# Optimization experiments

Measured on AMD Instinct MI355X. Metric: run time of the kernel, lower is better.

Reference implementation:

```python
import jax, jax.numpy as jnp
import numpy as np

EPS_LN = 1e-6
EPS_BN = 1e-5
NUM_HEADS = 8


def _dwconv(img, w, b=None, stride=1):
    # img: (B,C,H,W), w: (C,1,k,k) depthwise
    out = jax.lax.conv_general_dilated(
        img, w, (stride, stride), 'SAME',
        feature_group_count=img.shape[1],
        dimension_numbers=('NCHW', 'OIHW', 'NCHW'))
    if b is not None:
        out = out + b[None, :, None, None]
    return out


def _layernorm(x, g, b):
    m = jnp.mean(x, axis=-1, keepdims=True)
    v = jnp.mean(jnp.square(x - m), axis=-1, keepdims=True)
    return (x - m) * jax.lax.rsqrt(v + EPS_LN) * g + b


def _hardswish(x):
    return x * jnp.clip(x + 3.0, 0.0, 6.0) * (1.0 / 6.0)


def _forward(img, domain_label, pe_dw_w, pe_pw_w, pe_bn_g, pe_bn_b, pe_bn_m, pe_bn_v,
             cpe_w, cpe_b, norm1_g, norm1_b, qkv_w, qkv_b,
             crpe_w3, crpe_b3, crpe_w5, crpe_b5, crpe_w7, crpe_b7,
             dom_w1, dom_b1, dom_w2, dom_b2, proj_w, proj_b,
             norm2_g, norm2_b, fc1_w, fc1_b, fc2_w, fc2_b, d):
    B = img.shape[0]
    # --- DWCPatchEmbed_M: depthwise 3x3 s2 + pointwise 1x1 + domain BN (eval) + hardswish ---
    x = _dwconv(img, pe_dw_w, None, stride=2)                      # (B,Cin,H,W)
    x = jax.lax.conv_general_dilated(x, pe_pw_w, (1, 1), 'SAME',
                                     dimension_numbers=('NCHW', 'OIHW', 'NCHW'))
    g, be, mu, var = pe_bn_g[d], pe_bn_b[d], pe_bn_m[d], pe_bn_v[d]
    scale_bn = g * jax.lax.rsqrt(var + EPS_BN)
    x = (x - mu[None, :, None, None]) * scale_bn[None, :, None, None] + be[None, :, None, None]
    x = _hardswish(x)
    _, C, H, W = x.shape
    N = H * W
    x = x.reshape(B, C, N).transpose(0, 2, 1)                      # (B,N,C) tokens

    # --- ConvPosEnc: depthwise 3x3 on image layout, residual ---
    img2 = x.transpose(0, 2, 1).reshape(B, C, H, W)
    x = x + _dwconv(img2, cpe_w, cpe_b).reshape(B, C, N).transpose(0, 2, 1)

    # --- FactorAtt_ConvRelPosEnc_Sup ---
    cur = _layernorm(x, norm1_g[d], norm1_b[d])
    h = NUM_HEADS
    Ch = C // h
    qkv = cur @ qkv_w + qkv_b                                      # (B,N,3C)
    qkv = qkv.reshape(B, N, 3, h, Ch).transpose(2, 0, 3, 1, 4)     # (3,B,h,N,Ch)
    q, k, v = qkv[0], qkv[1], qkv[2]
    k_sm = jax.nn.softmax(k, axis=2)                               # softmax over tokens
    kv = jnp.einsum('bhnk,bhnv->bhkv', k_sm, v)                    # (B,h,Ch,Ch)
    factor_att = jnp.einsum('bhnk,bhkv->bhnv', q, kv)              # (B,h,N,Ch)

    # conv relative position encoding: windows {3:2heads, 5:3heads, 7:3heads}
    v_img = v.transpose(0, 1, 3, 2).reshape(B, C, H, W)            # (B, h*Ch, H, W)
    s1, s2 = 2 * Ch, 5 * Ch
    cv = jnp.concatenate([
        _dwconv(v_img[:, :s1], crpe_w3, crpe_b3),
        _dwconv(v_img[:, s1:s2], crpe_w5, crpe_b5),
        _dwconv(v_img[:, s2:], crpe_w7, crpe_b7)], axis=1)
    cv = cv.reshape(B, h, Ch, N).transpose(0, 1, 3, 2)             # (B,h,N,Ch)
    crpe = q * cv

    factor_att = (Ch ** -0.5) * factor_att + crpe

    # domain gate: Linear->ReLU->Linear on one-hot, softmax over heads
    da = jax.nn.relu(domain_label @ dom_w1 + dom_b1) @ dom_w2 + dom_b2   # (B,C)
    da = da.reshape(B, h, Ch)[:, :, None, :]                        # (B,h,1,Ch)
    da = jax.nn.softmax(da, axis=1)
    out = da * factor_att                                           # (B,h,N,Ch)
    out = out.transpose(0, 2, 1, 3).reshape(B, N, C)
    out = out @ proj_w + proj_b
    x = x + out

    # --- MLP (ratio 8), domain LayerNorm, residual ---
    cur = _layernorm(x, norm2_g[d], norm2_b[d])
    cur = jax.nn.gelu(cur @ fc1_w + fc1_b, approximate=False) @ fc2_w + fc2_b
    x = x + cur
    return x


def setup_inputs() -> dict:
    key = jax.random.key(0)
    ks = jax.random.split(key, 16)
    B, Cin, Hin, Win = 8, 64, 128, 128
    C, h, D = 128, NUM_HEADS, 4
    Ch = C // h
    hid_dom = C // 2
    hid_mlp = 8 * C
    f = jnp.float32

    def n(k, shape, s=0.02):
        return (s * jax.random.normal(k, shape)).astype(f)

    img = jax.random.normal(ks[0], (B, Cin, Hin, Win), dtype=f)
    domain_label = jax.nn.one_hot(jnp.zeros((B,), jnp.int32), D, dtype=f)
    return dict(
        img=img, domain_label=domain_label,
        pe_dw_w=n(ks[1], (Cin, 1, 3, 3), 0.1),
        pe_pw_w=n(ks[2], (C, Cin, 1, 1), 0.1),
        pe_bn_g=jnp.ones((D, C), f), pe_bn_b=jnp.zeros((D, C), f),
        pe_bn_m=n(ks[3], (D, C), 0.1),
        pe_bn_v=jnp.ones((D, C), f),
        cpe_w=n(ks[4], (C, 1, 3, 3), 0.1), cpe_b=jnp.zeros((C,), f),
        norm1_g=jnp.ones((D, C), f), norm1_b=jnp.zeros((D, C), f),
        qkv_w=n(ks[5], (C, 3 * C)), qkv_b=jnp.zeros((3 * C,), f),
        crpe_w3=n(ks[6], (2 * Ch, 1, 3, 3), 0.1), crpe_b3=jnp.zeros((2 * Ch,), f),
        crpe_w5=n(ks[7], (3 * Ch, 1, 5, 5), 0.1), crpe_b5=jnp.zeros((3 * Ch,), f),
        crpe_w7=n(ks[8], (3 * Ch, 1, 7, 7), 0.1), crpe_b7=jnp.zeros((3 * Ch,), f),
        dom_w1=n(ks[9], (D, hid_dom)), dom_b1=jnp.zeros((hid_dom,), f),
        dom_w2=n(ks[10], (hid_dom, C)), dom_b2=jnp.zeros((C,), f),
        proj_w=n(ks[11], (C, C)), proj_b=jnp.zeros((C,), f),
        norm2_g=jnp.ones((D, C), f), norm2_b=jnp.zeros((D, C), f),
        fc1_w=n(ks[12], (C, hid_mlp)), fc1_b=jnp.zeros((hid_mlp,), f),
        fc2_w=n(ks[13], (hid_mlp, C)), fc2_b=jnp.zeros((C,), f),
        d=0,
    )


def reference(img, domain_label, pe_dw_w, pe_pw_w, pe_bn_g, pe_bn_b, pe_bn_m, pe_bn_v,
              cpe_w, cpe_b, norm1_g, norm1_b, qkv_w, qkv_b,
              crpe_w3, crpe_b3, crpe_w5, crpe_b5, crpe_w7, crpe_b7,
              dom_w1, dom_b1, dom_w2, dom_b2, proj_w, proj_b,
              norm2_g, norm2_b, fc1_w, fc1_b, fc2_w, fc2_b, d):
    return _forward(img, domain_label, pe_dw_w, pe_pw_w, pe_bn_g, pe_bn_b, pe_bn_m, pe_bn_v,
                    cpe_w, cpe_b, norm1_g, norm1_b, qkv_w, qkv_b,
                    crpe_w3, crpe_b3, crpe_w5, crpe_b5, crpe_w7, crpe_b7,
                    dom_w1, dom_b1, dom_w2, dom_b2, proj_w, proj_b,
                    norm2_g, norm2_b, fc1_w, fc1_b, fc2_w, fc2_b, d)
```

## Files before the change

kernel.cpp:

```cpp
#include <hip/hip_runtime.h>
#include <math.h>

#define EPS_LN 1e-6f
#define EPS_BN 1e-5f

typedef __attribute__((ext_vector_type(8))) short bf16x8;
typedef __attribute__((ext_vector_type(4))) float f32x4;

__device__ __forceinline__ float wave_reduce_sum(float v) {
    #pragma unroll
    for (int m = 32; m >= 1; m >>= 1) v += __shfl_xor(v, m, 64);
    return v;
}
__device__ __forceinline__ float wave_reduce_max(float v) {
    #pragma unroll
    for (int m = 32; m >= 1; m >>= 1) v = fmaxf(v, __shfl_xor(v, m, 64));
    return v;
}
__device__ __forceinline__ short f2bf(float f) {
    union { float f; unsigned u; } v; v.f = f;
    unsigned r = v.u + 0x7fff + ((v.u >> 16) & 1);
    return (short)(r >> 16);
}
__device__ __forceinline__ unsigned pack2bf(float a, float b) {
    return (unsigned)(unsigned short)f2bf(a) | ((unsigned)(unsigned short)f2bf(b) << 16);
}

__global__ __launch_bounds__(256) void pe_kernel(
    const float* __restrict__ img, const float* __restrict__ dww,
    const float* __restrict__ pww, const float* __restrict__ bn_g,
    const float* __restrict__ bn_b, const float* __restrict__ bn_m,
    const float* __restrict__ bn_v, const int* __restrict__ dptr,
    float* __restrict__ t1) {
    __shared__ float dw[64 * 68];
    __shared__ float wsm[64 * 132];
    int bx = blockIdx.x;
    int b = bx >> 6, y = bx & 63;
    int tid = threadIdx.x;
    int d = *dptr;

    for (int idx = tid; idx < 8192; idx += 256) {
        int co = idx >> 6, ci = idx & 63;
        wsm[ci * 132 + co] = pww[idx];
    }

    for (int it = 0; it < 4; ++it) {
        int task = tid + it * 256;
        int ci = task >> 4, xx0 = (task & 15) * 4;
        const float* ip = img + (size_t)(b * 64 + ci) * 16384;
        const float* wd = dww + ci * 9;
        float a0 = 0.f, a1 = 0.f, a2 = 0.f, a3 = 0.f;
        #pragma unroll
        for (int r = 0; r < 3; ++r) {
            int iy = 2 * y + r;
            if (iy >= 128) continue;
            const float* rp = ip + iy * 128 + 2 * xx0;
            float u[9];
            *(f32x4*)&u[0] = *(const f32x4*)rp;
            *(f32x4*)&u[4] = *(const f32x4*)(rp + 4);
            u[8] = (xx0 < 60) ? rp[8] : 0.f;
            #pragma unroll
            for (int s = 0; s < 3; ++s) {
                float w = wd[r * 3 + s];
                a0 += u[s] * w;
                a1 += u[2 + s] * w;
                a2 += u[4 + s] * w;
                a3 += u[6 + s] * w;
            }
        }
        f32x4 st = {a0, a1, a2, a3};
        *(f32x4*)&dw[ci * 68 + xx0] = st;
    }
    __syncthreads();

    int xg = tid & 15, cog = tid >> 4;
    int xx0 = xg * 4, co0 = cog * 8;
    f32x4 acc[8];
    f32x4 zr = {0.f, 0.f, 0.f, 0.f};
    #pragma unroll
    for (int i = 0; i < 8; ++i) acc[i] = zr;
    for (int ci = 0; ci < 64; ++ci) {
        f32x4 dv = *(const f32x4*)&dw[ci * 68 + xx0];
        f32x4 w0 = *(const f32x4*)&wsm[ci * 132 + co0];
        f32x4 w1 = *(const f32x4*)&wsm[ci * 132 + co0 + 4];
        acc[0] += dv * w0.x; acc[1] += dv * w0.y;
        acc[2] += dv * w0.z; acc[3] += dv * w0.w;
        acc[4] += dv * w1.x; acc[5] += dv * w1.y;
        acc[6] += dv * w1.z; acc[7] += dv * w1.w;
    }
    #pragma unroll
    for (int i = 0; i < 8; ++i) {
        int co = co0 + i;
        float sc = bn_g[d * 128 + co] * rsqrtf(bn_v[d * 128 + co] + EPS_BN);
        float mu = bn_m[d * 128 + co], be = bn_b[d * 128 + co];
        f32x4 v = (acc[i] - mu) * sc + be;
        f32x4 r;
        r.x = v.x * fminf(fmaxf(v.x + 3.f, 0.f), 6.f) * (1.f / 6.f);
        r.y = v.y * fminf(fmaxf(v.y + 3.f, 0.f), 6.f) * (1.f / 6.f);
        r.z = v.z * fminf(fmaxf(v.z + 3.f, 0.f), 6.f) * (1.f / 6.f);
        r.w = v.w * fminf(fmaxf(v.w + 3.f, 0.f), 6.f) * (1.f / 6.f);
        *(f32x4*)&t1[(size_t)(b * 128 + co) * 4096 + y * 64 + xx0] = r;
    }
}

__global__ __launch_bounds__(256) void cpe_kernel(
    const float* __restrict__ t1, const float* __restrict__ cw,
    const float* __restrict__ cb, float* __restrict__ xout) {
    int bx = blockIdx.x;
    int cq = bx & 3, y = (bx >> 2) & 63, b = bx >> 8;
    int c0 = cq * 32;
    __shared__ float s[3 * 32 * 65];
    int tid = threadIdx.x;
    for (int idx = tid; idx < 3 * 32 * 64; idx += 256) {
        int xx = idx & 63;
        int cl = (idx >> 6) & 31;
        int dy = idx >> 11;
        int yy = y + dy - 1;
        float v = 0.f;
        if (yy >= 0 && yy < 64)
            v = t1[(size_t)(b * 128 + c0 + cl) * 4096 + yy * 64 + xx];
        s[(dy * 32 + cl) * 65 + xx] = v;
    }
    __syncthreads();
    for (int idx = tid; idx < 32 * 64; idx += 256) {
        int cl = idx & 31;
        int xx = idx >> 5;
        int c = c0 + cl;
        float center = s[(32 + cl) * 65 + xx];
        float acc = cb[c];
        #pragma unroll
        for (int dy = 0; dy < 3; ++dy) {
            #pragma unroll
            for (int dx = 0; dx < 3; ++dx) {
                int sx = xx + dx - 1;
                if (sx < 0 || sx >= 64) continue;
                acc += s[(dy * 32 + cl) * 65 + sx] * cw[c * 9 + dy * 3 + dx];
            }
        }
        xout[(size_t)(b * 4096 + y * 64 + xx) * 128 + c] = center + acc;
    }
}

__global__ __launch_bounds__(256) void pack_qkv_kernel(
    const float* __restrict__ w, const float* __restrict__ g,
    const int* __restrict__ dptr, short* __restrict__ wp) {
    int idx = blockIdx.x * 256 + threadIdx.x;
    int d = *dptr;
    int l = idx & 63, kk = (idx >> 6) & 3, n = idx >> 8;
    int k0 = kk * 32 + (l >> 4) * 8;
    int c = n * 16 + (l & 15);
    bf16x8 v;
    #pragma unroll
    for (int j = 0; j < 8; ++j)
        v[j] = f2bf(g[d * 128 + k0 + j] * w[(size_t)(k0 + j) * 384 + c]);
    *(bf16x8*)&wp[(size_t)idx * 8] = v;
}
__global__ __launch_bounds__(256) void pack_pw_kernel(
    const float* __restrict__ w, short* __restrict__ wp) {
    int idx = blockIdx.x * 256 + threadIdx.x;
    int l = idx & 63, kk = (idx >> 6) & 3, n = idx >> 8;
    int k0 = kk * 32 + (l >> 4) * 8;
    int c = n * 16 + (l & 15);
    bf16x8 v;
    #pragma unroll
    for (int j = 0; j < 8; ++j) v[j] = f2bf(w[(size_t)(k0 + j) * 128 + c]);
    *(bf16x8*)&wp[(size_t)idx * 8] = v;
}
__global__ __launch_bounds__(256) void pack_w1_kernel(
    const float* __restrict__ w1, const float* __restrict__ g,
    const int* __restrict__ dptr, short* __restrict__ w1p) {
    int idx = blockIdx.x * 256 + threadIdx.x;
    int d = *dptr;
    int l = idx & 63, kk = (idx >> 6) & 3, n = idx >> 8;
    int k0 = kk * 32 + (l >> 4) * 8;
    int c = n * 16 + (l & 15);
    bf16x8 v;
    #pragma unroll
    for (int j = 0; j < 8; ++j)
        v[j] = f2bf(g[d * 128 + k0 + j] * w1[(size_t)(k0 + j) * 1024 + c]);
    *(bf16x8*)&w1p[(size_t)idx * 8] = v;
}
__global__ __launch_bounds__(256) void pack_w2_kernel(
    const float* __restrict__ w2, short* __restrict__ w2p) {
    int idx = blockIdx.x * 256 + threadIdx.x;
    int l = idx & 63, kk = (idx >> 6) & 31, n = idx >> 11;
    int k0 = kk * 32 + (l >> 4) * 8;
    int c = n * 16 + (l & 15);
    bf16x8 v;
    #pragma unroll
    for (int j = 0; j < 8; ++j) v[j] = f2bf(w2[(size_t)(k0 + j) * 128 + c]);
    *(bf16x8*)&w2p[(size_t)idx * 8] = v;
}

__global__ __launch_bounds__(256) void fold_qkv_bias_kernel(
    const float* __restrict__ w, const float* __restrict__ bqkv,
    const float* __restrict__ beta, const int* __restrict__ dptr,
    float* __restrict__ bp) {
    int j = blockIdx.x * 256 + threadIdx.x;
    if (j >= 384) return;
    int d = *dptr;
    float s = bqkv[j];
    for (int k = 0; k < 128; ++k) s += beta[d * 128 + k] * w[(size_t)k * 384 + j];
    bp[j] = s;
}
__global__ __launch_bounds__(256) void fold_fc1_bias_kernel(
    const float* __restrict__ w, const float* __restrict__ b1,
    const float* __restrict__ beta, const int* __restrict__ dptr,
    float* __restrict__ bp) {
    int j = blockIdx.x * 256 + threadIdx.x;
    if (j >= 1024) return;
    int d = *dptr;
    float s = b1[j];
    for (int k = 0; k < 128; ++k) s += beta[d * 128 + k] * w[(size_t)k * 1024 + j];
    bp[j] = s;
}

__global__ __launch_bounds__(512, 4) void qkv_mfma_kernel(
    const float* __restrict__ x, const short* __restrict__ wp,
    const float* __restrict__ biasp, float* __restrict__ q_img,
    float* __restrict__ k_img, float* __restrict__ v_img) {
    int tb = blockIdx.x * 32;
    int tid = threadIdx.x;
    int lane = tid & 63, wv = tid >> 6;
    int tt = wv & 1, g = wv >> 1;
    int lhi = lane >> 4, llo = lane & 15;
    int b = tb >> 12, n0 = tb & 4095;

    bf16x8 afr[4];
    {
        f32x4 v0[4], v1[4];
        float sum = 0.f;
        #pragma unroll
        for (int kk = 0; kk < 4; ++kk) {
            const float* p = x + (size_t)(tb + tt * 16 + llo) * 128 + kk * 32 + lhi * 8;
            v0[kk] = *(const f32x4*)p;
            v1[kk] = *(const f32x4*)(p + 4);
            sum += v0[kk].x + v0[kk].y + v0[kk].z + v0[kk].w
                 + v1[kk].x + v1[kk].y + v1[kk].z + v1[kk].w;
        }
        sum += __shfl_xor(sum, 16, 64);
        sum += __shfl_xor(sum, 32, 64);
        float mean = sum * (1.f / 128.f);
        float vs = 0.f;
        #pragma unroll
        for (int kk = 0; kk < 4; ++kk) {
            f32x4 a = v0[kk], c = v1[kk];
            float d0 = a.x - mean, d1 = a.y - mean, d2 = a.z - mean, d3 = a.w - mean;
            float d4 = c.x - mean, d5 = c.y - mean, d6 = c.z - mean, d7 = c.w - mean;
            vs += d0*d0 + d1*d1 + d2*d2 + d3*d3 + d4*d4 + d5*d5 + d6*d6 + d7*d7;
        }
        vs += __shfl_xor(vs, 16, 64);
        vs += __shfl_xor(vs, 32, 64);
        float rs = rsqrtf(vs * (1.f / 128.f) + EPS_LN);
        #pragma unroll
        for (int kk = 0; kk < 4; ++kk) {
            bf16x8 o;
            o[0] = f2bf((v0[kk].x - mean) * rs);
            o[1] = f2bf((v0[kk].y - mean) * rs);
            o[2] = f2bf((v0[kk].z - mean) * rs);
            o[3] = f2bf((v0[kk].w - mean) * rs);
            o[4] = f2bf((v1[kk].x - mean) * rs);
            o[5] = f2bf((v1[kk].y - mean) * rs);
            o[6] = f2bf((v1[kk].z - mean) * rs);
            o[7] = f2bf((v1[kk].w - mean) * rs);
            afr[kk] = o;
        }
    }

    f32x4 acc[6];
    f32x4 zr = {0.f, 0.f, 0.f, 0.f};
    #pragma unroll
    for (int i = 0; i < 6; ++i) acc[i] = zr;

    #pragma unroll
    for (int i = 0; i < 6; ++i) {
        int nb = g * 6 + i;
        #pragma unroll
        for (int kk = 0; kk < 4; ++kk) {
            bf16x8 wf = *(const bf16x8*)&wp[((size_t)(nb * 4 + kk) * 64 + lane) * 8];
            acc[i] = __builtin_amdgcn_mfma_f32_16x16x32_bf16(wf, afr[kk], acc[i], 0, 0, 0);
        }
    }

    #pragma unroll
    for (int i = 0; i < 6; ++i) {
        int j0 = (g * 6 + i) * 16;
        f32x4 bv = *(const f32x4*)(biasp + j0 + lhi * 4);
        float* dst = (j0 < 128) ? q_img : ((j0 < 256) ? k_img : v_img);
        int c0 = (j0 & 127) + lhi * 4;
        f32x4 r = acc[i] + bv;
        float* p = dst + (size_t)(b * 128 + c0) * 4096 + n0 + tt * 16 + llo;
        p[0]        = r.x;
        p[4096]     = r.y;
        p[2 * 4096] = r.z;
        p[3 * 4096] = r.w;
    }
}

__global__ __launch_bounds__(256) void softmax_kernel(float* __restrict__ k_img) {
    __shared__ float red[4];
    float* p = k_img + (size_t)blockIdx.x * 4096;
    int tid = threadIdx.x;
    float v[16];
    float mx = -1e30f;
    #pragma unroll
    for (int i = 0; i < 16; ++i) {
        v[i] = p[tid + i * 256];
        mx = fmaxf(mx, v[i]);
    }
    mx = wave_reduce_max(mx);
    int wid = tid >> 6, lane = tid & 63;
    if (lane == 0) red[wid] = mx;
    __syncthreads();
    mx = fmaxf(fmaxf(red[0], red[1]), fmaxf(red[2], red[3]));
    __syncthreads();
    float sum = 0.f;
    #pragma unroll
    for (int i = 0; i < 16; ++i) {
        v[i] = expf(v[i] - mx);
        sum += v[i];
    }
    sum = wave_reduce_sum(sum);
    if (lane == 0) red[wid] = sum;
    __syncthreads();
    float inv = 1.f / (red[0] + red[1] + red[2] + red[3]);
    #pragma unroll
    for (int i = 0; i < 16; ++i)
        p[tid + i * 256] = v[i] * inv;
}

__global__ __launch_bounds__(256) void kv_part_kernel(
    const float* __restrict__ k_img, const float* __restrict__ v_img,
    float* __restrict__ kvp) {
    __shared__ float ks[16 * 132], vs[16 * 132];
    int bc = blockIdx.x;
    int bh = bc >> 3, chunk = bc & 7;
    int b = bh >> 3, h = bh & 7;
    int tid = threadIdx.x;
    int ck = tid >> 4, cv = tid & 15;
    float acc = 0.f;
    const float* kp = k_img + (size_t)(b * 128 + h * 16) * 4096;
    const float* vp = v_img + (size_t)(b * 128 + h * 16) * 4096;
    int nb0 = chunk * 512;
    for (int nb = nb0; nb < nb0 + 512; nb += 128) {
        for (int idx = tid; idx < 2048; idx += 256) {
            int r = idx >> 7, col = idx & 127;
            ks[r * 132 + col] = kp[(size_t)r * 4096 + nb + col];
            vs[r * 132 + col] = vp[(size_t)r * 4096 + nb + col];
        }
        __syncthreads();
        for (int kk = 0; kk < 128; ++kk)
            acc += ks[ck * 132 + kk] * vs[cv * 132 + kk];
        __syncthreads();
    }
    kvp[(size_t)(chunk * 64 + bh) * 256 + ck * 16 + cv] = acc;
}
__global__ __launch_bounds__(256) void kv_reduce_kernel(
    const float* __restrict__ kvp, float* __restrict__ kv) {
    int i = blockIdx.x * 256 + threadIdx.x;
    float s = 0.f;
    #pragma unroll
    for (int c = 0; c < 8; ++c) s += kvp[(size_t)c * 16384 + i];
    kv[i] = s;
}

__global__ __launch_bounds__(256) void fa_kernel(
    const float* __restrict__ q_img, const float* __restrict__ kv,
    float* __restrict__ fa_img) {
    __shared__ float kvs[256];
    int bid = blockIdx.x;
    int bh = bid >> 4, chunk = bid & 15;
    int b = bh >> 3, h = bh & 7;
    int tid = threadIdx.x;
    kvs[tid] = kv[bh * 256 + tid];
    __syncthreads();
    int n = chunk * 256 + tid;
    const float* qp = q_img + (size_t)(b * 128 + h * 16) * 4096 + n;
    float qv[16];
    #pragma unroll
    for (int ck = 0; ck < 16; ++ck) qv[ck] = qp[(size_t)ck * 4096];
    float* fp = fa_img + (size_t)(b * 128 + h * 16) * 4096 + n;
    #pragma unroll
    for (int cv = 0; cv < 16; ++cv) {
        float s = 0.f;
        #pragma unroll
        for (int ck = 0; ck < 16; ++ck) s += qv[ck] * kvs[ck * 16 + cv];
        fp[(size_t)cv * 4096] = s;
    }
}

__global__ __launch_bounds__(256) void gate_kernel(
    const float* __restrict__ dl, const float* __restrict__ w1,
    const float* __restrict__ b1, const float* __restrict__ w2,
    const float* __restrict__ b2, float* __restrict__ da) {
    __shared__ float hid[512];
    __shared__ float raw[1024];
    int tid = threadIdx.x;
    for (int idx = tid; idx < 512; idx += 256) {
        int b = idx >> 6, jj = idx & 63;
        float a = b1[jj];
        #pragma unroll
        for (int dd = 0; dd < 4; ++dd)
            a += dl[b * 4 + dd] * w1[dd * 64 + jj];
        hid[idx] = fmaxf(a, 0.f);
    }
    __syncthreads();
    for (int idx = tid; idx < 1024; idx += 256) {
        int b = idx >> 7, c = idx & 127;
        float a = b2[c];
        for (int jj = 0; jj < 64; ++jj)
            a += hid[b * 64 + jj] * w2[jj * 128 + c];
        raw[idx] = a;
    }
    __syncthreads();
    if (tid < 128) {
        int b = tid >> 4, ch = tid & 15;
        float mx = -1e30f;
        #pragma unroll
        for (int hh = 0; hh < 8; ++hh)
            mx = fmaxf(mx, raw[b * 128 + hh * 16 + ch]);
        float e[8];
        float s = 0.f;
        #pragma unroll
        for (int hh = 0; hh < 8; ++hh) {
            e[hh] = expf(raw[b * 128 + hh * 16 + ch] - mx);
            s += e[hh];
        }
        float inv = 1.f / s;
        #pragma unroll
        for (int hh = 0; hh < 8; ++hh)
            da[b * 128 + hh * 16 + ch] = e[hh] * inv;
    }
}

template<int KC>
__device__ __forceinline__ void conv4(const float* __restrict__ s,
                                      const float* __restrict__ wsm,
                                      int y, int xx0, float* a4) {
    const int OFF = KC / 2;
    #pragma unroll
    for (int dy = 0; dy < KC; ++dy) {
        int sy = y + dy - OFF;
        if (sy < 0 || sy >= 64) continue;
        const float* r = s + sy * 72;
        float u[12];
        *(f32x4*)&u[0] = *(const f32x4*)&r[xx0];
        *(f32x4*)&u[4] = *(const f32x4*)&r[xx0 + 4];
        *(f32x4*)&u[8] = *(const f32x4*)&r[xx0 + 8];
        #pragma unroll
        for (int dx = 0; dx < KC; ++dx) {
            float w = wsm[dy * KC + dx];
            const int base = dx - OFF + 4;
            a4[0] += u[base + 0] * w;
            a4[1] += u[base + 1] * w;
            a4[2] += u[base + 2] * w;
            a4[3] += u[base + 3] * w;
        }
    }
}

__global__ __launch_bounds__(256) void att_kernel(
    const float* __restrict__ q_img, const float* __restrict__ v_img,
    const float* __restrict__ fa_img, const float* __restrict__ da,
    const float* __restrict__ w3, const float* __restrict__ b3,
    const float* __restrict__ w5, const float* __restrict__ b5,
    const float* __restrict__ w7, const float* __restrict__ b7,
    float* __restrict__ att) {
    __shared__ float s[64 * 72];
    __shared__ float wsm[49];
    int o = ((blockIdx.x & 7) << 7) | (blockIdx.x >> 3);
    int b = o >> 7, c = o & 127;
    int tid = threadIdx.x;
    const float* vp = v_img + (size_t)(b * 128 + c) * 4096;
    for (int idx = tid; idx < 4096; idx += 256) {
        int row = idx >> 6, xx = idx & 63;
        s[row * 72 + xx + 4] = vp[idx];
    }
    for (int idx = tid; idx < 512; idx += 256) {
        int row = idx >> 3, j = idx & 7;
        s[row * 72 + (j < 4 ? j : 64 + j)] = 0.f;
    }
    int kc; const float* wp; float bias;
    if (c < 32)      { kc = 3; wp = w3 + c * 9;         bias = b3[c]; }
    else if (c < 80) { kc = 5; wp = w5 + (c - 32) * 25; bias = b5[c - 32]; }
    else             { kc = 7; wp = w7 + (c - 80) * 49; bias = b7[c - 80]; }
    if (tid < kc * kc) wsm[tid] = wp[tid];
    float dac = da[b * 128 + c];
    size_t rowbase = (size_t)(b * 128 + c) * 4096;
    __syncthreads();
    for (int it = 0; it < 4; ++it) {
        int task = tid + it * 256;
        int y = task >> 4, xx0 = (task & 15) * 4;
        float a4[4] = {bias, bias, bias, bias};
        if (kc == 3)      conv4<3>(s, wsm, y, xx0, a4);
        else if (kc == 5) conv4<5>(s, wsm, y, xx0, a4);
        else              conv4<7>(s, wsm, y, xx0, a4);
        size_t base = rowbase + y * 64 + xx0;
        f32x4 fav = *(const f32x4*)&fa_img[base];
        f32x4 qv  = *(const f32x4*)&q_img[base];
        f32x4 cv4 = {a4[0], a4[1], a4[2], a4[3]};
        f32x4 r = (fav * 0.25f + qv * cv4) * dac;
        *(f32x4*)&att[base] = r;
    }
}

__global__ __launch_bounds__(256, 2) void proj_mfma_kernel(
    const float* __restrict__ att, const short* __restrict__ wp,
    const float* __restrict__ bias, const float* __restrict__ xres,
    float* __restrict__ out) {
    __shared__ float As[128 * 33];
    int tb = blockIdx.x * 32;
    int tid = threadIdx.x;
    int lane = tid & 63, wv = tid >> 6;
    int lhi = lane >> 4, llo = lane & 15;
    int b = tb >> 12, n0 = tb & 4095;

    for (int idx = tid; idx < 4096; idx += 256) {
        int c = idx >> 5, t = idx & 31;
        As[c * 33 + t] = att[(size_t)(b * 128 + c) * 4096 + n0 + t];
    }
    __syncthreads();

    bf16x8 afr[2][4];
    #pragma unroll
    for (int tt = 0; tt < 2; ++tt) {
        #pragma unroll
        for (int kk = 0; kk < 4; ++kk) {
            int c0 = kk * 32 + lhi * 8;
            int t = tt * 16 + llo;
            bf16x8 v;
            #pragma unroll
            for (int j = 0; j < 8; ++j) v[j] = f2bf(As[(c0 + j) * 33 + t]);
            afr[tt][kk] = v;
        }
    }

    f32x4 acc[2][2];
    f32x4 zr = {0.f, 0.f, 0.f, 0.f};
    #pragma unroll
    for (int i = 0; i < 2; ++i) { acc[i][0] = zr; acc[i][1] = zr; }

    #pragma unroll
    for (int i = 0; i < 2; ++i) {
        int nb = wv * 2 + i;
        #pragma unroll
        for (int kk = 0; kk < 4; ++kk) {
            bf16x8 wf = *(const bf16x8*)&wp[((size_t)(nb * 4 + kk) * 64 + lane) * 8];
            acc[i][0] = __builtin_amdgcn_mfma_f32_16x16x32_bf16(wf, afr[0][kk], acc[i][0], 0, 0, 0);
            acc[i][1] = __builtin_amdgcn_mfma_f32_16x16x32_bf16(wf, afr[1][kk], acc[i][1], 0, 0, 0);
        }
    }

    #pragma unroll
    for (int i = 0; i < 2; ++i) {
        int j0 = (wv * 2 + i) * 16;
        f32x4 bv = *(const f32x4*)(bias + j0 + lhi * 4);
        #pragma unroll
        for (int tt = 0; tt < 2; ++tt) {
            size_t o = (size_t)(tb + tt * 16 + llo) * 128 + j0 + lhi * 4;
            f32x4 xr = *(const f32x4*)(xres + o);
            *(f32x4*)(out + o) = xr + acc[i][tt] + bv;
        }
    }
}

__global__ __launch_bounds__(512, 4) void mlp_mfma_kernel(
    const short* __restrict__ w1p, const float* __restrict__ b1p,
    const short* __restrict__ w2p, const float* __restrict__ b2,
    float* io) {
    __shared__ short hs[32768];
    int tb = blockIdx.x * 32;
    int tid = threadIdx.x;
    int lane = tid & 63, wv = tid >> 6;
    int tt = wv & 1, g = wv >> 1;
    int lhi = lane >> 4, llo = lane & 15;

    bf16x8 afr[4];
    {
        f32x4 v0[4], v1[4];
        float sum = 0.f;
        #pragma unroll
        for (int kk = 0; kk < 4; ++kk) {
            const float* p = io + (size_t)(tb + tt * 16 + llo) * 128 + kk * 32 + lhi * 8;
            v0[kk] = *(const f32x4*)p;
            v1[kk] = *(const f32x4*)(p + 4);
            sum += v0[kk].x + v0[kk].y + v0[kk].z + v0[kk].w
                 + v1[kk].x + v1[kk].y + v1[kk].z + v1[kk].w;
        }
        sum += __shfl_xor(sum, 16, 64);
        sum += __shfl_xor(sum, 32, 64);
        float mean = sum * (1.f / 128.f);
        float vs = 0.f;
        #pragma unroll
        for (int kk = 0; kk < 4; ++kk) {
            f32x4 a = v0[kk], c = v1[kk];
            float d0 = a.x - mean, d1 = a.y - mean, d2 = a.z - mean, d3 = a.w - mean;
            float d4 = c.x - mean, d5 = c.y - mean, d6 = c.z - mean, d7 = c.w - mean;
            vs += d0*d0 + d1*d1 + d2*d2 + d3*d3 + d4*d4 + d5*d5 + d6*d6 + d7*d7;
        }
        vs += __shfl_xor(vs, 16, 64);
        vs += __shfl_xor(vs, 32, 64);
        float rs = rsqrtf(vs * (1.f / 128.f) + EPS_LN);
        #pragma unroll
        for (int kk = 0; kk < 4; ++kk) {
            bf16x8 o;
            o[0] = f2bf((v0[kk].x - mean) * rs);
            o[1] = f2bf((v0[kk].y - mean) * rs);
            o[2] = f2bf((v0[kk].z - mean) * rs);
            o[3] = f2bf((v0[kk].w - mean) * rs);
            o[4] = f2bf((v1[kk].x - mean) * rs);
            o[5] = f2bf((v1[kk].y - mean) * rs);
            o[6] = f2bf((v1[kk].z - mean) * rs);
            o[7] = f2bf((v1[kk].w - mean) * rs);
            afr[kk] = o;
        }
    }

    f32x4 acc[16];
    f32x4 zr = {0.f, 0.f, 0.f, 0.f};
    #pragma unroll
    for (int nl = 0; nl < 16; ++nl) acc[nl] = zr;

    const short* wbase = w1p + (size_t)(g * 16) * 4 * 64 * 8;
    #pragma unroll
    for (int nl = 0; nl < 16; ++nl) {
        #pragma unroll
        for (int kk = 0; kk < 4; ++kk) {
            bf16x8 bf = *(const bf16x8*)(wbase + ((size_t)(nl * 4 + kk) * 64 + lane) * 8);
            acc[nl] = __builtin_amdgcn_mfma_f32_16x16x32_bf16(bf, afr[kk], acc[nl], 0, 0, 0);
        }
    }

    #pragma unroll
    for (int nl = 0; nl < 16; ++nl) {
        int hn = g * 16 + nl;
        int hc0 = hn * 16 + lhi * 4;
        f32x4 bv = *(const f32x4*)(b1p + hc0);
        int kk2 = hn >> 1;
        int lp = llo + 16 * ((hn & 1) * 2 + (lhi >> 1));
        f32x4 a = acc[nl] + bv;
        float g0 = 0.5f * a.x * (1.f + erff(a.x * 0.70710678118654752f));
        float g1 = 0.5f * a.y * (1.f + erff(a.y * 0.70710678118654752f));
        float g2 = 0.5f * a.z * (1.f + erff(a.z * 0.70710678118654752f));
        float g3 = 0.5f * a.w * (1.f + erff(a.w * 0.70710678118654752f));
        uint2 wv2;
        wv2.x = pack2bf(g0, g1);
        wv2.y = pack2bf(g2, g3);
        *(uint2*)((char*)hs + ((size_t)(tt * 32 + kk2) * 64 + lp) * 16 + (lhi & 1) * 8) = wv2;
    }
    __syncthreads();

    f32x4 acc2[2];
    acc2[0] = zr; acc2[1] = zr;

    const short* w2base = w2p + (size_t)wv * 32 * 64 * 8;
    #pragma unroll 4
    for (int kk2 = 0; kk2 < 32; ++kk2) {
        bf16x8 h0 = *(const bf16x8*)&hs[((size_t)(0 * 32 + kk2) * 64 + lane) * 8];
        bf16x8 h1 = *(const bf16x8*)&hs[((size_t)(1 * 32 + kk2) * 64 + lane) * 8];
        bf16x8 w0 = *(const bf16x8*)(w2base + ((size_t)kk2 * 64 + lane) * 8);
        acc2[0] = __builtin_amdgcn_mfma_f32_16x16x32_bf16(w0, h0, acc2[0], 0, 0, 0);
        acc2[1] = __builtin_amdgcn_mfma_f32_16x16x32_bf16(w0, h1, acc2[1], 0, 0, 0);
    }

    int c0 = wv * 16 + lhi * 4;
    f32x4 bv = *(const f32x4*)(b2 + c0);
    #pragma unroll
    for (int tt2 = 0; tt2 < 2; ++tt2) {
        float* op = io + (size_t)(tb + tt2 * 16 + llo) * 128 + c0;
        f32x4 r = *(f32x4*)op;
        r = r + acc2[tt2] + bv;
        *(f32x4*)op = r;
    }
}

extern "C" void kernel_launch(void* const* d_in, const int* in_sizes, int n_in,
                              void* d_out, int out_size, void* d_ws, size_t ws_size,
                              hipStream_t stream) {
    const float* img   = (const float*)d_in[0];
    const float* dl    = (const float*)d_in[1];
    const float* pe_dw = (const float*)d_in[2];
    const float* pe_pw = (const float*)d_in[3];
    const float* bn_g  = (const float*)d_in[4];
    const float* bn_b  = (const float*)d_in[5];
    const float* bn_m  = (const float*)d_in[6];
    const float* bn_v  = (const float*)d_in[7];
    const float* cpe_w = (const float*)d_in[8];
    const float* cpe_b = (const float*)d_in[9];
    const float* n1_g  = (const float*)d_in[10];
    const float* n1_b  = (const float*)d_in[11];
    const float* qkv_w = (const float*)d_in[12];
    const float* qkv_b = (const float*)d_in[13];
    const float* w3    = (const float*)d_in[14];
    const float* b3    = (const float*)d_in[15];
    const float* w5    = (const float*)d_in[16];
    const float* b5    = (const float*)d_in[17];
    const float* w7    = (const float*)d_in[18];
    const float* b7    = (const float*)d_in[19];
    const float* dw1   = (const float*)d_in[20];
    const float* db1   = (const float*)d_in[21];
    const float* dw2   = (const float*)d_in[22];
    const float* db2   = (const float*)d_in[23];
    const float* pw    = (const float*)d_in[24];
    const float* pb    = (const float*)d_in[25];
    const float* n2_g  = (const float*)d_in[26];
    const float* n2_b  = (const float*)d_in[27];
    const float* f1w   = (const float*)d_in[28];
    const float* f1b   = (const float*)d_in[29];
    const float* f2w   = (const float*)d_in[30];
    const float* f2b   = (const float*)d_in[31];
    const int*   dptr  = (const int*)d_in[32];
    float* out = (float*)d_out;

    char* ws = (char*)d_ws;
    const size_t SZ = (size_t)8 * 128 * 4096 * 4;
    float* t1    = (float*)(ws);
    float* x     = (float*)(ws + SZ);
    float* q_img = (float*)(ws + 2 * SZ);
    float* k_img = (float*)(ws + 3 * SZ);
    float* v_img = (float*)(ws + 4 * SZ);
    float* kv    = (float*)(ws + 5 * SZ);
    float* da    = (float*)(ws + 5 * SZ + 0x10000);
    short* qkvp  = (short*)(ws + 5 * SZ + 0x20000);
    short* pwp   = (short*)(ws + 5 * SZ + 0x40000);
    float* qbp   = (float*)(ws + 5 * SZ + 0x48000);
    float* f1bp  = (float*)(ws + 5 * SZ + 0x4A000);
    float* kvp   = (float*)(ws + 5 * SZ + 0x50000);
    float* fa_img = t1;
    short* w1p   = (short*)(ws + 2 * SZ);
    short* w2p   = (short*)(ws + 2 * SZ + 262144);

    pack_qkv_kernel<<<24, 256, 0, stream>>>(qkv_w, n1_g, dptr, qkvp);
    fold_qkv_bias_kernel<<<2, 256, 0, stream>>>(qkv_w, qkv_b, n1_b, dptr, qbp);
    pack_pw_kernel<<<8, 256, 0, stream>>>(pw, pwp);
    gate_kernel<<<1, 256, 0, stream>>>(dl, dw1, db1, dw2, db2, da);
    pe_kernel<<<512, 256, 0, stream>>>(img, pe_dw, pe_pw, bn_g, bn_b, bn_m, bn_v, dptr, t1);
    cpe_kernel<<<2048, 256, 0, stream>>>(t1, cpe_w, cpe_b, x);
    qkv_mfma_kernel<<<1024, 512, 0, stream>>>(x, qkvp, qbp, q_img, k_img, v_img);
    softmax_kernel<<<1024, 256, 0, stream>>>(k_img);
    kv_part_kernel<<<512, 256, 0, stream>>>(k_img, v_img, kvp);
    kv_reduce_kernel<<<64, 256, 0, stream>>>(kvp, kv);
    fa_kernel<<<1024, 256, 0, stream>>>(q_img, kv, fa_img);
    att_kernel<<<1024, 256, 0, stream>>>(q_img, v_img, fa_img, da, w3, b3, w5, b5, w7, b7, k_img);
    proj_mfma_kernel<<<1024, 256, 0, stream>>>(k_img, pwp, pb, x, out);
    pack_w1_kernel<<<64, 256, 0, stream>>>(f1w, n2_g, dptr, w1p);
    fold_fc1_bias_kernel<<<4, 256, 0, stream>>>(f1w, f1b, n2_b, dptr, f1bp);
    pack_w2_kernel<<<64, 256, 0, stream>>>(f2w, w2p);
    mlp_mfma_kernel<<<1024, 512, 0, stream>>>(w1p, f1bp, w2p, f2b, out);
}
```

Baseline: 367.6 us.

## Merge prep kernels, fold kv reduce into fa, retile MLP and use fast GELU

The six weight-packing and bias-folding kernels and the gate kernel are merged into one prep kernel, cutting launch count. The kv partial reduction moves into fa_kernel, which removes one more launch and one round trip through global memory. The MLP kernel changes its split so each wave covers both token tiles over 8 hidden blocks, reusing each loaded weight fragment for two MFMAs, and launch bounds drop to 3 blocks per SM. Exact erf GELU is replaced by a sigmoid-form tanh approximation, which is cheaper but numerically different.

```diff
diff --git a/kernel.cpp b/kernel.cpp
--- a/kernel.cpp
+++ b/kernel.cpp
@@ -24,6 +24,12 @@
 }
 __device__ __forceinline__ unsigned pack2bf(float a, float b) {
     return (unsigned)(unsigned short)f2bf(a) | ((unsigned)(unsigned short)f2bf(b) << 16);
+}
+__device__ __forceinline__ float gelu_f(float x) {
+    float x2 = x * x;
+    float u = x * (-1.595769122f - 0.071354816f * x2) * 1.0f;
+    float e = __expf(u);
+    return x * __builtin_amdgcn_rcpf(1.f + e);
 }
 
 __global__ __launch_bounds__(256) void pe_kernel(
@@ -141,78 +147,114 @@
     }
 }
 
-__global__ __launch_bounds__(256) void pack_qkv_kernel(
-    const float* __restrict__ w, const float* __restrict__ g,
-    const int* __restrict__ dptr, short* __restrict__ wp) {
-    int idx = blockIdx.x * 256 + threadIdx.x;
+__global__ __launch_bounds__(256) void prep_kernel(
+    const float* __restrict__ qkv_w, const float* __restrict__ n1_g,
+    const float* __restrict__ n1_b, const float* __restrict__ qkv_b,
+    const float* __restrict__ pw, const float* __restrict__ f1w,
+    const float* __restrict__ n2_g, const float* __restrict__ n2_b,
+    const float* __restrict__ f1b, const float* __restrict__ f2w,
+    const float* __restrict__ dl, const float* __restrict__ dw1,
+    const float* __restrict__ db1, const float* __restrict__ dw2,
+    const float* __restrict__ db2, const int* __restrict__ dptr,
+    short* __restrict__ qkvp, short* __restrict__ pwp,
+    short* __restrict__ w1p, short* __restrict__ w2p,
+    float* __restrict__ qbp, float* __restrict__ f1bp,
+    float* __restrict__ da) {
+    __shared__ float sh[1536];
+    int bb = blockIdx.x;
+    int tid = threadIdx.x;
     int d = *dptr;
-    int l = idx & 63, kk = (idx >> 6) & 3, n = idx >> 8;
-    int k0 = kk * 32 + (l >> 4) * 8;
-    int c = n * 16 + (l & 15);
-    bf16x8 v;
-    #pragma unroll
-    for (int j = 0; j < 8; ++j)
-        v[j] = f2bf(g[d * 128 + k0 + j] * w[(size_t)(k0 + j) * 384 + c]);
-    *(bf16x8*)&wp[(size_t)idx * 8] = v;
-}
-__global__ __launch_bounds__(256) void pack_pw_kernel(
-    const float* __restrict__ w, short* __restrict__ wp) {
-    int idx = blockIdx.x * 256 + threadIdx.x;
-    int l = idx & 63, kk = (idx >> 6) & 3, n = idx >> 8;
-    int k0 = kk * 32 + (l >> 4) * 8;
-    int c = n * 16 + (l & 15);
-    bf16x8 v;
-    #pragma unroll
-    for (int j = 0; j < 8; ++j) v[j] = f2bf(w[(size_t)(k0 + j) * 128 + c]);
-    *(bf16x8*)&wp[(size_t)idx * 8] = v;
-}
-__global__ __launch_bounds__(256) void pack_w1_kernel(
-    const float* __restrict__ w1, const float* __restrict__ g,
-    const int* __restrict__ dptr, short* __restrict__ w1p) {
-    int idx = blockIdx.x * 256 + threadIdx.x;
-    int d = *dptr;
-    int l = idx & 63, kk = (idx >> 6) & 3, n = idx >> 8;
-    int k0 = kk * 32 + (l >> 4) * 8;
-    int c = n * 16 + (l & 15);
-    bf16x8 v;
-    #pragma unroll
-    for (int j = 0; j < 8; ++j)
-        v[j] = f2bf(g[d * 128 + k0 + j] * w1[(size_t)(k0 + j) * 1024 + c]);
-    *(bf16x8*)&w1p[(size_t)idx * 8] = v;
-}
-__global__ __launch_bounds__(256) void pack_w2_kernel(
-    const float* __restrict__ w2, short* __restrict__ w2p) {
-    int idx = blockIdx.x * 256 + threadIdx.x;
-    int l = idx & 63, kk = (idx >> 6) & 31, n = idx >> 11;
-    int k0 = kk * 32 + (l >> 4) * 8;
-    int c = n * 16 + (l & 15);
-    bf16x8 v;
-    #pragma unroll
-    for (int j = 0; j < 8; ++j) v[j] = f2bf(w2[(size_t)(k0 + j) * 128 + c]);
-    *(bf16x8*)&w2p[(size_t)idx * 8] = v;
-}
-
-__global__ __launch_bounds__(256) void fold_qkv_bias_kernel(
-    const float* __restrict__ w, const float* __restrict__ bqkv,
-    const float* __restrict__ beta, const int* __restrict__ dptr,
-    float* __restrict__ bp) {
-    int j = blockIdx.x * 256 + threadIdx.x;
-    if (j >= 384) return;
-    int d = *dptr;
-    float s = bqkv[j];
-    for (int k = 0; k < 128; ++k) s += beta[d * 128 + k] * w[(size_t)k * 384 + j];
-    bp[j] = s;
-}
-__global__ __launch_bounds__(256) void fold_fc1_bias_kernel(
-    const float* __restrict__ w, const float* __restrict__ b1,
-    const float* __restrict__ beta, const int* __restrict__ dptr,
-    float* __restrict__ bp) {
-    int j = blockIdx.x * 256 + threadIdx.x;
-    if (j >= 1024) return;
-    int d = *dptr;
-    float s = b1[j];
-    for (int k = 0; k < 128; ++k) s += beta[d * 128 + k] * w[(size_t)k * 1024 + j];
-    bp[j] = s;
+    if (bb < 24) {
+        int idx = bb * 256 + tid;
+        int l = idx & 63, kk = (idx >> 6) & 3, n = idx >> 8;
+        int k0 = kk * 32 + (l >> 4) * 8;
+        int c = n * 16 + (l & 15);
+        bf16x8 v;
+        #pragma unroll
+        for (int j = 0; j < 8; ++j)
+            v[j] = f2bf(n1_g[d * 128 + k0 + j] * qkv_w[(size_t)(k0 + j) * 384 + c]);
+        *(bf16x8*)&qkvp[(size_t)idx * 8] = v;
+    } else if (bb < 32) {
+        int idx = (bb - 24) * 256 + tid;
+        int l = idx & 63, kk = (idx >> 6) & 3, n = idx >> 8;
+        int k0 = kk * 32 + (l >> 4) * 8;
+        int c = n * 16 + (l & 15);
+        bf16x8 v;
+        #pragma unroll
+        for (int j = 0; j < 8; ++j) v[j] = f2bf(pw[(size_t)(k0 + j) * 128 + c]);
+        *(bf16x8*)&pwp[(size_t)idx * 8] = v;
+    } else if (bb < 96) {
+        int idx = (bb - 32) * 256 + tid;
+        int l = idx & 63, kk = (idx >> 6) & 3, n = idx >> 8;
+        int k0 = kk * 32 + (l >> 4) * 8;
+        int c = n * 16 + (l & 15);
+        bf16x8 v;
+        #pragma unroll
+        for (int j = 0; j < 8; ++j)
+            v[j] = f2bf(n2_g[d * 128 + k0 + j] * f1w[(size_t)(k0 + j) * 1024 + c]);
+        *(bf16x8*)&w1p[(size_t)idx * 8] = v;
+    } else if (bb < 160) {
+        int idx = (bb - 96) * 256 + tid;
+        int l = idx & 63, kk = (idx >> 6) & 31, n = idx >> 11;
+        int k0 = kk * 32 + (l >> 4) * 8;
+        int c = n * 16 + (l & 15);
+        bf16x8 v;
+        #pragma unroll
+        for (int j = 0; j < 8; ++j) v[j] = f2bf(f2w[(size_t)(k0 + j) * 128 + c]);
+        *(bf16x8*)&w2p[(size_t)idx * 8] = v;
+    } else if (bb < 162) {
+        int j = (bb - 160) * 256 + tid;
+        if (j < 384) {
+            float s = qkv_b[j];
+            for (int k = 0; k < 128; ++k)
+                s += n1_b[d * 128 + k] * qkv_w[(size_t)k * 384 + j];
+            qbp[j] = s;
+        }
+    } else if (bb < 166) {
+        int j = (bb - 162) * 256 + tid;
+        float s = f1b[j];
+        for (int k = 0; k < 128; ++k)
+            s += n2_b[d * 128 + k] * f1w[(size_t)k * 1024 + j];
+        f1bp[j] = s;
+    } else {
+        float* hid = sh;
+        float* raw = sh + 512;
+        for (int idx = tid; idx < 512; idx += 256) {
+            int b = idx >> 6, jj = idx & 63;
+            float a = db1[jj];
+            #pragma unroll
+            for (int dd = 0; dd < 4; ++dd)
+                a += dl[b * 4 + dd] * dw1[dd * 64 + jj];
+            hid[idx] = fmaxf(a, 0.f);
+        }
+        __syncthreads();
+        for (int idx = tid; idx < 1024; idx += 256) {
+            int b = idx >> 7, c = idx & 127;
+            float a = db2[c];
+            for (int jj = 0; jj < 64; ++jj)
+                a += hid[b * 64 + jj] * dw2[jj * 128 + c];
+            raw[idx] = a;
+        }
+        __syncthreads();
+        if (tid < 128) {
+            int b = tid >> 4, ch = tid & 15;
+            float mx = -1e30f;
+            #pragma unroll
+            for (int hh = 0; hh < 8; ++hh)
+                mx = fmaxf(mx, raw[b * 128 + hh * 16 + ch]);
+            float e[8];
+            float s = 0.f;
+            #pragma unroll
+            for (int hh = 0; hh < 8; ++hh) {
+                e[hh] = expf(raw[b * 128 + hh * 16 + ch] - mx);
+                s += e[hh];
+            }
+            float inv = 1.f / s;
+            #pragma unroll
+            for (int hh = 0; hh < 8; ++hh)
+                da[b * 128 + hh * 16 + ch] = e[hh] * inv;
+        }
+    }
 }
 
 __global__ __launch_bounds__(512, 4) void qkv_mfma_kernel(
@@ -355,24 +397,21 @@
     }
     kvp[(size_t)(chunk * 64 + bh) * 256 + ck * 16 + cv] = acc;
 }
-__global__ __launch_bounds__(256) void kv_reduce_kernel(
-    const float* __restrict__ kvp, float* __restrict__ kv) {
-    int i = blockIdx.x * 256 + threadIdx.x;
-    float s = 0.f;
-    #pragma unroll
-    for (int c = 0; c < 8; ++c) s += kvp[(size_t)c * 16384 + i];
-    kv[i] = s;
-}
 
 __global__ __launch_bounds__(256) void fa_kernel(
-    const float* __restrict__ q_img, const float* __restrict__ kv,
+    const float* __restrict__ q_img, const float* __restrict__ kvp,
     float* __restrict__ fa_img) {
     __shared__ float kvs[256];
     int bid = blockIdx.x;
     int bh = bid >> 4, chunk = bid & 15;
     int b = bh >> 3, h = bh & 7;
     int tid = threadIdx.x;
-    kvs[tid] = kv[bh * 256 + tid];
+    {
+        float s = 0.f;
+        #pragma unroll
+        for (int c = 0; c < 8; ++c) s += kvp[(size_t)c * 16384 + bh * 256 + tid];
+        kvs[tid] = s;
+    }
     __syncthreads();
     int n = chunk * 256 + tid;
     const float* qp = q_img + (size_t)(b * 128 + h * 16) * 4096 + n;
@@ -386,50 +425,6 @@
         #pragma unroll
         for (int ck = 0; ck < 16; ++ck) s += qv[ck] * kvs[ck * 16 + cv];
         fp[(size_t)cv * 4096] = s;
-    }
-}
-
-__global__ __launch_bounds__(256) void gate_kernel(
-    const float* __restrict__ dl, const float* __restrict__ w1,
-    const float* __restrict__ b1, const float* __restrict__ w2,
-    const float* __restrict__ b2, float* __restrict__ da) {
-    __shared__ float hid[512];
-    __shared__ float raw[1024];
-    int tid = threadIdx.x;
-    for (int idx = tid; idx < 512; idx += 256) {
-        int b = idx >> 6, jj = idx & 63;
-        float a = b1[jj];
-        #pragma unroll
-        for (int dd = 0; dd < 4; ++dd)
-            a += dl[b * 4 + dd] * w1[dd * 64 + jj];
-        hid[idx] = fmaxf(a, 0.f);
-    }
-    __syncthreads();
-    for (int idx = tid; idx < 1024; idx += 256) {
-        int b = idx >> 7, c = idx & 127;
-        float a = b2[c];
-        for (int jj = 0; jj < 64; ++jj)
-            a += hid[b * 64 + jj] * w2[jj * 128 + c];
-        raw[idx] = a;
-    }
-    __syncthreads();
-    if (tid < 128) {
-        int b = tid >> 4, ch = tid & 15;
-        float mx = -1e30f;
-        #pragma unroll
-        for (int hh = 0; hh < 8; ++hh)
-            mx = fmaxf(mx, raw[b * 128 + hh * 16 + ch]);
-        float e[8];
-        float s = 0.f;
-        #pragma unroll
-        for (int hh = 0; hh < 8; ++hh) {
-            e[hh] = expf(raw[b * 128 + hh * 16 + ch] - mx);
-            s += e[hh];
-        }
-        float inv = 1.f / s;
-        #pragma unroll
-        for (int hh = 0; hh < 8; ++hh)
-            da[b * 128 + hh * 16 + ch] = e[hh] * inv;
     }
 }
 
@@ -564,7 +559,7 @@
     }
 }
 
-__global__ __launch_bounds__(512, 4) void mlp_mfma_kernel(
+__global__ __launch_bounds__(512, 3) void mlp_mfma_kernel(
     const short* __restrict__ w1p, const float* __restrict__ b1p,
     const short* __restrict__ w2p, const float* __restrict__ b2,
     float* io) {
@@ -572,11 +567,11 @@
     int tb = blockIdx.x * 32;
     int tid = threadIdx.x;
     int lane = tid & 63, wv = tid >> 6;
-    int tt = wv & 1, g = wv >> 1;
     int lhi = lane >> 4, llo = lane & 15;
 
-    bf16x8 afr[4];
-    {
+    bf16x8 afr[2][4];
+    #pragma unroll
+    for (int tt = 0; tt < 2; ++tt) {
         f32x4 v0[4], v1[4];
         float sum = 0.f;
         #pragma unroll
@@ -612,41 +607,43 @@
             o[5] = f2bf((v1[kk].y - mean) * rs);
             o[6] = f2bf((v1[kk].z - mean) * rs);
             o[7] = f2bf((v1[kk].w - mean) * rs);
-            afr[kk] = o;
-        }
-    }
-
-    f32x4 acc[16];
+            afr[tt][kk] = o;
+        }
+    }
+
+    f32x4 acc[2][8];
     f32x4 zr = {0.f, 0.f, 0.f, 0.f};
     #pragma unroll
-    for (int nl = 0; nl < 16; ++nl) acc[nl] = zr;
-
-    const short* wbase = w1p + (size_t)(g * 16) * 4 * 64 * 8;
-    #pragma unroll
-    for (int nl = 0; nl < 16; ++nl) {
+    for (int tt = 0; tt < 2; ++tt)
+        #pragma unroll
+        for (int nl = 0; nl < 8; ++nl) acc[tt][nl] = zr;
+
+    const short* wbase = w1p + (size_t)(wv * 8) * 4 * 64 * 8;
+    #pragma unroll
+    for (int nl = 0; nl < 8; ++nl) {
         #pragma unroll
         for (int kk = 0; kk < 4; ++kk) {
             bf16x8 bf = *(const bf16x8*)(wbase + ((size_t)(nl * 4 + kk) * 64 + lane) * 8);
-            acc[nl] = __builtin_amdgcn_mfma_f32_16x16x32_bf16(bf, afr[kk], acc[nl], 0, 0, 0);
-        }
-    }
-
-    #pragma unroll
-    for (int nl = 0; nl < 16; ++nl) {
-        int hn = g * 16 + nl;
+            acc[0][nl] = __builtin_amdgcn_mfma_f32_16x16x32_bf16(bf, afr[0][kk], acc[0][nl], 0, 0, 0);
+            acc[1][nl] = __builtin_amdgcn_mfma_f32_16x16x32_bf16(bf, afr[1][kk], acc[1][nl], 0, 0, 0);
+        }
+    }
+
+    #pragma unroll
+    for (int nl = 0; nl < 8; ++nl) {
+        int hn = wv * 8 + nl;
         int hc0 = hn * 16 + lhi * 4;
         f32x4 bv = *(const f32x4*)(b1p + hc0);
         int kk2 = hn >> 1;
         int lp = llo + 16 * ((hn & 1) * 2 + (lhi >> 1));
-        f32x4 a = acc[nl] + bv;
-        float g0 = 0.5f * a.x * (1.f + erff(a.x * 0.70710678118654752f));
-        float g1 = 0.5f * a.y * (1.f + erff(a.y * 0.70710678118654752f));
-        float g2 = 0.5f * a.z * (1.f + erff(a.z * 0.70710678118654752f));
-        float g3 = 0.5f * a.w * (1.f + erff(a.w * 0.70710678118654752f));
-        uint2 wv2;
-        wv2.x = pack2bf(g0, g1);
-        wv2.y = pack2bf(g2, g3);
-        *(uint2*)((char*)hs + ((size_t)(tt * 32 + kk2) * 64 + lp) * 16 + (lhi & 1) * 8) = wv2;
+        #pragma unroll
+        for (int tt = 0; tt < 2; ++tt) {
+            f32x4 a = acc[tt][nl] + bv;
+            uint2 wv2;
+            wv2.x = pack2bf(gelu_f(a.x), gelu_f(a.y));
+            wv2.y = pack2bf(gelu_f(a.z), gelu_f(a.w));
+            *(uint2*)((char*)hs + ((size_t)(tt * 32 + kk2) * 64 + lp) * 16 + (lhi & 1) * 8) = wv2;
+        }
     }
     __syncthreads();
 
@@ -719,32 +716,27 @@
     float* q_img = (float*)(ws + 2 * SZ);
     float* k_img = (float*)(ws + 3 * SZ);
     float* v_img = (float*)(ws + 4 * SZ);
-    float* kv    = (float*)(ws + 5 * SZ);
     float* da    = (float*)(ws + 5 * SZ + 0x10000);
     short* qkvp  = (short*)(ws + 5 * SZ + 0x20000);
     short* pwp   = (short*)(ws + 5 * SZ + 0x40000);
     float* qbp   = (float*)(ws + 5 * SZ + 0x48000);
     float* f1bp  = (float*)(ws + 5 * SZ + 0x4A000);
     float* kvp   = (float*)(ws + 5 * SZ + 0x50000);
+    short* w1p   = (short*)(ws + 5 * SZ + 0xD0000);
+    short* w2p   = (short*)(ws + 5 * SZ + 0x110000);
     float* fa_img = t1;
-    short* w1p   = (short*)(ws + 2 * SZ);
-    short* w2p   = (short*)(ws + 2 * SZ + 262144);
-
-    pack_qkv_kernel<<<24, 256, 0, stream>>>(qkv_w, n1_g, dptr, qkvp);
-    fold_qkv_bias_kernel<<<2, 256, 0, stream>>>(qkv_w, qkv_b, n1_b, dptr, qbp);
-    pack_pw_kernel<<<8, 256, 0, stream>>>(pw, pwp);
-    gate_kernel<<<1, 256, 0, stream>>>(dl, dw1, db1, dw2, db2, da);
+
+    prep_kernel<<<167, 256, 0, stream>>>(qkv_w, n1_g, n1_b, qkv_b, pw, f1w,
+                                         n2_g, n2_b, f1b, f2w, dl, dw1, db1,
+                                         dw2, db2, dptr, qkvp, pwp, w1p, w2p,
+                                         qbp, f1bp, da);
     pe_kernel<<<512, 256, 0, stream>>>(img, pe_dw, pe_pw, bn_g, bn_b, bn_m, bn_v, dptr, t1);
     cpe_kernel<<<2048, 256, 0, stream>>>(t1, cpe_w, cpe_b, x);
     qkv_mfma_kernel<<<1024, 512, 0, stream>>>(x, qkvp, qbp, q_img, k_img, v_img);
     softmax_kernel<<<1024, 256, 0, stream>>>(k_img);
     kv_part_kernel<<<512, 256, 0, stream>>>(k_img, v_img, kvp);
-    kv_reduce_kernel<<<64, 256, 0, stream>>>(kvp, kv);
-    fa_kernel<<<1024, 256, 0, stream>>>(q_img, kv, fa_img);
+    fa_kernel<<<1024, 256, 0, stream>>>(q_img, kvp, fa_img);
     att_kernel<<<1024, 256, 0, stream>>>(q_img, v_img, fa_img, da, w3, b3, w5, b5, w7, b7, k_img);
     proj_mfma_kernel<<<1024, 256, 0, stream>>>(k_img, pwp, pb, x, out);
-    pack_w1_kernel<<<64, 256, 0, stream>>>(f1w, n2_g, dptr, w1p);
-    fold_fc1_bias_kernel<<<4, 256, 0, stream>>>(f1w, f1b, n2_b, dptr, f1bp);
-    pack_w2_kernel<<<64, 256, 0, stream>>>(f2w, w2p);
     mlp_mfma_kernel<<<1024, 512, 0, stream>>>(w1p, f1bp, w2p, f2b, out);
 }
```

Result: faster. 337.9 us (-8.1%).
